# Performance work log

Measured on AMD Instinct MI355X. Metric: run time of the kernel, lower is better.

The kernel has to match this reference:

```python
import jax, jax.numpy as jnp
import numpy as np

B, T, H = 8, 2048, 2048

def glorot(key, shape):
    return jax.random.uniform(key, shape, minval=-1.0, maxval=1.0) * jnp.sqrt(2 / sum(shape))

def setup_inputs() -> dict:
    key = jax.random.key(0)
    kx, kr, ka, kb = jax.random.split(key, 4)
    x_seq = jax.random.normal(kx, (B, T, H), dtype=jnp.float32)
    reset = jax.random.randint(kr, (B, T), 0, 2).astype(bool)
    a_mat = glorot(ka, (H, H))
    b_mat = glorot(kb, (H, H))
    return {"x_seq": x_seq, "reset": reset, "a_mat": a_mat, "b_mat": b_mat}

def reference(x_seq, reset, a_mat, b_mat):
    # Precompute B^T x_t for all timesteps in one big GEMM: (B^T x)_k = sum_h b[h,k] x[h]
    bx = jnp.einsum('hk,bth->btk', b_mat, x_seq)  # [B,T,H]
    bx_t = jnp.swapaxes(bx, 0, 1)                 # [T,B,H] time-major
    reset_t = jnp.swapaxes(reset, 0, 1)           # [T,B]

    def step(h, inp):
        bx_step, r = inp                          # [B,H], [B]
        h = jnp.where(r[:, None], 0.0, h)         # reset hidden state
        h = h @ a_mat.T + bx_step                 # A @ h per batch row
        return h, h

    h0 = jnp.zeros((B, H), dtype=x_seq.dtype)
    _, h_seq = jax.lax.scan(step, h0, (bx_t, reset_t))
    return jnp.swapaxes(h_seq, 0, 1)              # [B,T,H]
```

## Files before the change

kernel.cpp:

```cpp
#include <hip/hip_runtime.h>

#define Hn 2048
#define Bn 8
#define Tn 2048
#define Cn 16
#define NCn (Tn / Cn)
#define M2n (NCn * Bn)

using f32x4 = __attribute__((ext_vector_type(4))) float;
using u32x4 = __attribute__((ext_vector_type(4))) unsigned int;
using us4   = __attribute__((ext_vector_type(4))) unsigned short;
using bf8   = __attribute__((ext_vector_type(8))) short;
using f4    = __attribute__((ext_vector_type(4))) float;

#define GLOAD16(g, l) __builtin_amdgcn_global_load_lds(                      \
    (const __attribute__((address_space(1))) void*)(g),                      \
    (__attribute__((address_space(3))) void*)(l), 16, 0, 0)

__device__ __forceinline__ unsigned short f2bf(float f) {
    unsigned u = __builtin_bit_cast(unsigned, f);
    u = u + 0x7fffu + ((u >> 16) & 1u);
    return (unsigned short)(u >> 16);
}
__device__ __forceinline__ float bf2f(unsigned short h) {
    unsigned u = ((unsigned)h) << 16;
    return __builtin_bit_cast(float, u);
}
__device__ __forceinline__ void split2f(float v, unsigned short& a, unsigned short& b) {
    a = f2bf(v);
    b = f2bf(v - bf2f(a));
}

__global__ __launch_bounds__(256) void k_reset_prep(const unsigned int* __restrict__ rin,
                                                    unsigned char* __restrict__ r8,
                                                    int* __restrict__ cut,
                                                    int* __restrict__ firstReset,
                                                    int* __restrict__ anyUncut,
                                                    int* __restrict__ perm,
                                                    int* __restrict__ iperm,
                                                    int* __restrict__ counts) {
    __shared__ int s_badInt, s_badFloat;
    __shared__ int hist[17], off[18], cur[17];
    if (threadIdx.x == 0) { s_badInt = 0; s_badFloat = 0; *anyUncut = 0; }
    if (threadIdx.x < 17) hist[threadIdx.x] = 0;
    __syncthreads();
    int badI = 0, badF = 0;
    for (int i = threadIdx.x; i < 4096; i += 256) {
        unsigned int v = rin[i];
        if (v > 1u) badI = 1;
        if (v != 0u && v != 0x3f800000u) badF = 1;
    }
    if (badI) atomicOr(&s_badInt, 1);
    if (badF) atomicOr(&s_badFloat, 1);
    __syncthreads();
    const int fmt = (!s_badInt) ? 0 : ((!s_badFloat) ? 1 : 2);
    const unsigned char* rb = (const unsigned char*)rin;
    const float* rf = (const float*)rin;
    for (int i = threadIdx.x; i < Bn * Tn; i += 256) {
        unsigned char v;
        if (fmt == 0)      v = (unsigned char)(rin[i] != 0u);
        else if (fmt == 1) v = (unsigned char)(rf[i] != 0.0f);
        else               v = (unsigned char)(rb[i] != 0);
        r8[i] = v;
    }
    __syncthreads();
    int anyU = 0;
    for (int m = threadIdx.x; m < M2n; m += 256) {
        int c = m / Bn, b = m % Bn;
        int fr = Cn;
        for (int j = 0; j < Cn; j++) {
            if (r8[b * Tn + c * Cn + j]) { fr = j; break; }
        }
        firstReset[m] = fr;
        int ct = (fr < Cn);
        cut[m] = ct;
        if (!ct && c < NCn - 1) anyU = 1;
        atomicAdd(&hist[fr], 1);
    }
    if (anyU) atomicOr(anyUncut, 1);
    __syncthreads();
    if (threadIdx.x == 0) {
        off[16] = 0;
        for (int v = 15; v >= 0; v--) off[v] = off[v + 1] + hist[v + 1];
        for (int v = 0; v < 17; v++) cur[v] = (v == 16) ? 0 : off[v];
        for (int j = 0; j < 16; j++) counts[j] = off[j];
    }
    __syncthreads();
    for (int m = threadIdx.x; m < M2n; m += 256) {
        int fr = firstReset[m];
        int pos = atomicAdd(&cur[fr], 1);
        perm[pos] = m;
        iperm[m] = pos;
    }
}

__global__ __launch_bounds__(256) void k_split_A2(const float* __restrict__ A,
                                                  unsigned short* __restrict__ a1,
                                                  unsigned short* __restrict__ a2) {
    size_t i = ((size_t)blockIdx.x * 256 + threadIdx.x) * 4;
    f32x4 v = *(const f32x4*)&A[i];
    us4 h1, h2;
#pragma unroll
    for (int e = 0; e < 4; e++) {
        unsigned short x1, x2;
        split2f(v[e], x1, x2);
        h1[e] = x1; h2[e] = x2;
    }
    *(us4*)&a1[i] = h1; *(us4*)&a2[i] = h2;
}

__global__ __launch_bounds__(256) void k_split_Bt(const float* __restrict__ Bm,
                                                  unsigned short* __restrict__ b1,
                                                  unsigned short* __restrict__ b2) {
    __shared__ float tile[64][65];
    const int k0 = blockIdx.y * 64, n0 = blockIdx.x * 64;
    const int c = threadIdx.x & 63, r4 = threadIdx.x >> 6;
#pragma unroll
    for (int i = 0; i < 16; i++) {
        int r = r4 * 16 + i;
        tile[r][c] = Bm[(size_t)(k0 + r) * Hn + n0 + c];
    }
    __syncthreads();
#pragma unroll
    for (int i = 0; i < 16; i++) {
        int r = r4 * 16 + i;
        float v = tile[c][r];
        unsigned short x1, x2;
        split2f(v, x1, x2);
        b1[(size_t)(n0 + r) * Hn + k0 + c] = x1;
        b2[(size_t)(n0 + r) * Hn + k0 + c] = x2;
    }
}

__global__ __launch_bounds__(256) void k_split_X(const float* __restrict__ X,
                                                 unsigned short* __restrict__ x1,
                                                 unsigned short* __restrict__ x2) {
    size_t i = ((size_t)blockIdx.x * 256 + threadIdx.x) * 4;
    f32x4 v = *(const f32x4*)&X[i];
    us4 h1, h2;
#pragma unroll
    for (int e = 0; e < 4; e++) {
        unsigned short a, b;
        split2f(v[e], a, b);
        h1[e] = a; h2[e] = b;
    }
    *(us4*)&x1[i] = h1; *(us4*)&x2[i] = h2;
}

template<int PREX>
__global__ __launch_bounds__(512) void k_gemm_p1(const unsigned short* __restrict__ X0,
                                                 const unsigned short* __restrict__ X1,
                                                 const unsigned short* __restrict__ B0,
                                                 const unsigned short* __restrict__ B1,
                                                 const float* __restrict__ Xf,
                                                 float* __restrict__ Out,
                                                 unsigned short* __restrict__ S0,
                                                 unsigned short* __restrict__ S1) {
    constexpr int BM = 256, BN = 128, LW = 32;
    __shared__ unsigned short ldsA[2 * BM * LW];
    __shared__ unsigned short ldsB[2 * BN * LW];
    const int tid = threadIdx.x;
    const int lane = tid & 63;
    const int wv = tid >> 6;
    const int wm = wv >> 1, wn = wv & 1;
    const int n0 = blockIdx.x * BN;
    const int m0 = blockIdx.y * BM;

    f4 acc[4][4];
#pragma unroll
    for (int fm = 0; fm < 4; fm++)
#pragma unroll
        for (int fn = 0; fn < 4; fn++) acc[fm][fn] = (f4){0.f, 0.f, 0.f, 0.f};

    const unsigned short* gA[4];
    unsigned short* lA[4];
    const float* gX[2];
    unsigned short* lX[2];
    const unsigned short* gB[2];
    unsigned short* lB[2];
    if constexpr (PREX) {
#pragma unroll
        for (int q = 0; q < 4; q++) {
            int u = tid + q * 512;
            int sp = u >> 10, row = (u >> 2) & 255, slot = u & 3;
            int g = slot ^ ((row >> 1) & 3);
            gA[q] = (sp ? X1 : X0) + (size_t)(m0 + row) * Hn + g * 8;
            lA[q] = &ldsA[u * 8];
        }
    } else {
#pragma unroll
        for (int q = 0; q < 2; q++) {
            int u = tid + q * 512;
            int row = u >> 2, slot = u & 3;
            int s = slot ^ ((row >> 1) & 3);
            gX[q] = Xf + (size_t)row * 0 + (size_t)(m0 + row) * Hn + slot * 8;
            lX[q] = &ldsA[row * LW + s * 8];
        }
    }
#pragma unroll
    for (int q = 0; q < 2; q++) {
        int u = tid + q * 512;
        int sp = u >> 9, row = (u >> 2) & 127, slot = u & 3;
        int g = slot ^ ((row >> 1) & 3);
        gB[q] = (sp ? B1 : B0) + (size_t)(n0 + row) * Hn + g * 8;
        lB[q] = &ldsB[u * 8];
    }
    const int sl = (lane >> 4) ^ ((lane >> 1) & 3);

    for (int k0 = 0; k0 < Hn; k0 += 32) {
        if constexpr (PREX) {
#pragma unroll
            for (int q = 0; q < 4; q++) {
                GLOAD16(gA[q], lA[q]);
                gA[q] += 32;
            }
        } else {
#pragma unroll
            for (int q = 0; q < 2; q++) {
                f32x4 va = *(const f32x4*)gX[q];
                f32x4 vb = *(const f32x4*)(gX[q] + 4);
                gX[q] += 32;
                us4 h1a, h2a, h1b, h2b;
#pragma unroll
                for (int e = 0; e < 4; e++) {
                    unsigned short p, r;
                    split2f(va[e], p, r); h1a[e] = p; h2a[e] = r;
                    split2f(vb[e], p, r); h1b[e] = p; h2b[e] = r;
                }
                *(us4*)lX[q] = h1a;
                *(us4*)(lX[q] + 4) = h1b;
                *(us4*)(lX[q] + BM * LW) = h2a;
                *(us4*)(lX[q] + BM * LW + 4) = h2b;
            }
        }
#pragma unroll
        for (int q = 0; q < 2; q++) {
            GLOAD16(gB[q], lB[q]);
            gB[q] += 32;
        }
        __syncthreads();

        bf8 af[2][4], bfr[2][4];
#pragma unroll
        for (int sp = 0; sp < 2; sp++)
#pragma unroll
            for (int f = 0; f < 4; f++)
                af[sp][f] = *(const bf8*)&ldsA[(sp * BM + wm * 64 + f * 16 + (lane & 15)) * LW + sl * 8];
#pragma unroll
        for (int sp = 0; sp < 2; sp++)
#pragma unroll
            for (int f = 0; f < 4; f++)
                bfr[sp][f] = *(const bf8*)&ldsB[(sp * BN + wn * 64 + f * 16 + (lane & 15)) * LW + sl * 8];

        const int pa[3] = {0, 0, 1};
        const int pb[3] = {0, 1, 0};
#pragma unroll
        for (int p = 0; p < 3; p++)
#pragma unroll
            for (int fm = 0; fm < 4; fm++)
#pragma unroll
                for (int fn = 0; fn < 4; fn++)
                    acc[fm][fn] = __builtin_amdgcn_mfma_f32_16x16x32_bf16(
                        af[pa[p]][fm], bfr[pb[p]][fn], acc[fm][fn], 0, 0, 0);
        __syncthreads();
    }

#pragma unroll
    for (int fm = 0; fm < 4; fm++)
#pragma unroll
        for (int r = 0; r < 4; r++) {
            int row = m0 + wm * 64 + fm * 16 + (lane >> 4) * 4 + r;
            int bb = row >> 11, t = row & 2047;
            int isC0 = ((t & 15) == 0);
            size_t ob = (size_t)row * Hn;
            size_t sb = (size_t)((t >> 4) * 8 + bb) * Hn;
#pragma unroll
            for (int fn = 0; fn < 4; fn++) {
                int n = n0 + wn * 64 + fn * 16 + (lane & 15);
                float v = acc[fm][fn][r];
                Out[ob + n] = v;
                if (isC0) {
                    unsigned short h1, h2;
                    split2f(v, h1, h2);
                    S0[sb + n] = h1; S1[sb + n] = h2;
                }
            }
        }
}

template<int PHASE>
__global__ __launch_bounds__(256) void k_gemm_s(const unsigned short* __restrict__ S0,
                                                const unsigned short* __restrict__ S1,
                                                const unsigned short* __restrict__ W0,
                                                const unsigned short* __restrict__ W1,
                                                float* __restrict__ Out,
                                                unsigned short* __restrict__ O0,
                                                unsigned short* __restrict__ O1,
                                                const unsigned char* __restrict__ r8v,
                                                const int* __restrict__ perm,
                                                const int* __restrict__ iperm,
                                                const int* __restrict__ counts,
                                                unsigned short* __restrict__ U0,
                                                unsigned short* __restrict__ U1,
                                                float* __restrict__ Hin,
                                                int j) {
    constexpr int BM = 64, BN = 64, BK = 64;
    __shared__ unsigned short ldsA[2 * BM * BK];
    __shared__ unsigned short ldsB[2 * BN * BK];
    const int tid = threadIdx.x;
    const int lane = tid & 63;
    const int wv = tid >> 6;
    const int wm = wv >> 1, wn = wv & 1;
    const int n0 = blockIdx.x * BN;
    const int m0 = blockIdx.y * BM;

    int cnt = 0;
    if constexpr (PHASE == 4) {
        cnt = counts[j];
        if (m0 >= cnt) return;
    }

    f4 acc[2][2];
#pragma unroll
    for (int fm = 0; fm < 2; fm++)
#pragma unroll
        for (int fn = 0; fn < 2; fn++) acc[fm][fn] = (f4){0.f, 0.f, 0.f, 0.f};

    const unsigned short* gA[4];
    unsigned short* lA[4];
    const unsigned short* gB[4];
    unsigned short* lB[4];
#pragma unroll
    for (int q = 0; q < 4; q++) {
        int u = tid + q * 256;
        int sp = u >> 9, row = (u >> 3) & 63, s = u & 7;
        int g = s ^ (row & 7);
        gA[q] = (sp ? S1 : S0) + (size_t)(m0 + row) * Hn + g * 8;
        lA[q] = &ldsA[u * 8];
        gB[q] = (sp ? W1 : W0) + (size_t)(n0 + row) * Hn + g * 8;
        lB[q] = &ldsB[u * 8];
    }

    for (int k0 = 0; k0 < Hn; k0 += BK) {
#pragma unroll
        for (int q = 0; q < 4; q++) {
            GLOAD16(gA[q], lA[q]);
            GLOAD16(gB[q], lB[q]);
            gA[q] += BK;
            gB[q] += BK;
        }
        __syncthreads();

        const int pa[3] = {0, 0, 1};
        const int pb[3] = {0, 1, 0};
#pragma unroll
        for (int h = 0; h < 2; h++) {
            const int sl = (h * 4 + (lane >> 4)) ^ (lane & 7);
            bf8 af[2][2], bfr[2][2];
#pragma unroll
            for (int sp = 0; sp < 2; sp++)
#pragma unroll
                for (int f = 0; f < 2; f++) {
                    af[sp][f] = *(const bf8*)&ldsA[(sp * BM + wm * 32 + f * 16 + (lane & 15)) * BK + sl * 8];
                    bfr[sp][f] = *(const bf8*)&ldsB[(sp * BN + wn * 32 + f * 16 + (lane & 15)) * BK + sl * 8];
                }
#pragma unroll
            for (int p = 0; p < 3; p++)
#pragma unroll
                for (int fm = 0; fm < 2; fm++)
#pragma unroll
                    for (int fn = 0; fn < 2; fn++)
                        acc[fm][fn] = __builtin_amdgcn_mfma_f32_16x16x32_bf16(
                            af[pa[p]][fm], bfr[pb[p]][fn], acc[fm][fn], 0, 0, 0);
        }
        __syncthreads();
    }

    if constexpr (PHASE == 2 || PHASE == 3) {
#pragma unroll
        for (int fm = 0; fm < 2; fm++)
#pragma unroll
            for (int r = 0; r < 4; r++) {
                int m = m0 + wm * 32 + fm * 16 + (lane >> 4) * 4 + r;
                int cch = m >> 3, bb = m & 7;
                int t = cch * Cn + j;
                int rfl = r8v[bb * Tn + t];
                size_t ob = ((size_t)bb * Tn + t) * (size_t)Hn;
                size_t sb = (size_t)m * Hn;
                int carry = 0;
                size_t ub = 0, hb = 0;
                if constexpr (PHASE == 3) {
                    carry = (m < M2n - 8);
                    if (carry) {
                        ub = (size_t)iperm[m + 8] * Hn;
                        hb = (size_t)(m + 8) * Hn;
                    }
                }
#pragma unroll
                for (int fn = 0; fn < 2; fn++) {
                    int n = n0 + wn * 32 + fn * 16 + (lane & 15);
                    float v = (rfl ? 0.0f : acc[fm][fn][r]) + Out[ob + n];
                    Out[ob + n] = v;
                    unsigned short h1, h2;
                    split2f(v, h1, h2);
                    O0[sb + n] = h1; O1[sb + n] = h2;
                    if constexpr (PHASE == 3) {
                        if (carry) {
                            U0[ub + n] = h1; U1[ub + n] = h2;
                            Hin[hb + n] = v;
                        }
                    }
                }
            }
    } else {
#pragma unroll
        for (int fm = 0; fm < 2; fm++)
#pragma unroll
            for (int r = 0; r < 4; r++) {
                int s = m0 + wm * 32 + fm * 16 + (lane >> 4) * 4 + r;
                int alive = (s < cnt);
                int m = perm[s];
                int cch = m >> 3, bb = m & 7;
                int t = cch * Cn + j;
                size_t ob = ((size_t)bb * Tn + t) * (size_t)Hn;
                size_t sb = (size_t)s * Hn;
#pragma unroll
                for (int fn = 0; fn < 2; fn++) {
                    int n = n0 + wn * 32 + fn * 16 + (lane & 15);
                    if (alive) {
                        float val = acc[fm][fn][r];
                        unsigned short h1, h2;
                        split2f(val, h1, h2);
                        O0[sb + n] = h1; O1[sb + n] = h2;
                        Out[ob + n] += val;
                    }
                }
            }
    }
}

__global__ __launch_bounds__(256) void k_zero_c0(const int* __restrict__ iperm,
                                                 unsigned short* __restrict__ U0,
                                                 unsigned short* __restrict__ U1,
                                                 float* __restrict__ Hin) {
    int b = blockIdx.x;
    int s = iperm[b];
    for (int n = threadIdx.x; n < Hn; n += 256) {
        U0[(size_t)s * Hn + n] = 0;
        U1[(size_t)s * Hn + n] = 0;
        Hin[(size_t)b * Hn + n] = 0.0f;
    }
}

__global__ __launch_bounds__(1024) void k_fallback(float* __restrict__ Hin,
                                                   const float* __restrict__ A,
                                                   const int* __restrict__ cut,
                                                   const int* __restrict__ anyUncut,
                                                   unsigned short* __restrict__ u1,
                                                   unsigned short* __restrict__ u2,
                                                   const int* __restrict__ iperm) {
    if (*anyUncut == 0) return;
    __shared__ float v0[Hn];
    __shared__ float v1[Hn];
    for (int c = 1; c < NCn; c++) {
        for (int b = 0; b < Bn; b++) {
            if (cut[(c - 1) * Bn + b]) continue;
            for (int n = threadIdx.x; n < Hn; n += 1024)
                v0[n] = Hin[((size_t)(c - 1) * Bn + b) * Hn + n];
            __syncthreads();
            for (int s = 0; s < Cn; s++) {
                float* pin = (s & 1) ? v1 : v0;
                float* pout = (s & 1) ? v0 : v1;
                for (int n = threadIdx.x; n < Hn; n += 1024) {
                    float accv = 0.0f;
                    const float* Ar = &A[(size_t)n * Hn];
                    for (int k = 0; k < Hn; k++) accv += pin[k] * Ar[k];
                    pout[n] = accv;
                }
                __syncthreads();
            }
            float* pres = (Cn & 1) ? v1 : v0;
            int mrow = c * Bn + b;
            size_t dst = (size_t)mrow * Hn;
            size_t sdst = (size_t)iperm[mrow] * Hn;
            for (int n = threadIdx.x; n < Hn; n += 1024) {
                float nv = Hin[dst + n] + pres[n];
                Hin[dst + n] = nv;
                unsigned short h1, h2;
                split2f(nv, h1, h2);
                u1[sdst + n] = h1; u2[sdst + n] = h2;
            }
            __syncthreads();
        }
    }
}

extern "C" void kernel_launch(void* const* d_in, const int* in_sizes, int n_in,
                              void* d_out, int out_size, void* d_ws, size_t ws_size,
                              hipStream_t stream) {
    const float* x = (const float*)d_in[0];
    const unsigned int* rst = (const unsigned int*)d_in[1];
    const float* Am = (const float*)d_in[2];
    const float* Bm = (const float*)d_in[3];
    float* Out = (float*)d_out;
    char* ws = (char*)d_ws;

    unsigned char* r8 = (unsigned char*)ws;
    int* cut = (int*)(ws + 16384);
    int* firstReset = (int*)(ws + 20480);
    int* perm = (int*)(ws + 24576);
    int* iperm = (int*)(ws + 28672);
    int* counts = (int*)(ws + 32768);
    int* anyUncut = (int*)(ws + 32832);
    unsigned short* a1 = (unsigned short*)(ws + 65536);
    unsigned short* a2 = a1 + 4194304;
    unsigned short* b1 = a2 + 4194304;
    unsigned short* b2 = b1 + 4194304;
    unsigned short* sP1 = b2 + 4194304;
    unsigned short* sP2 = sP1 + 2097152;
    unsigned short* sQ1 = sP2 + 2097152;
    unsigned short* sQ2 = sQ1 + 2097152;
    unsigned short* uP1 = sQ2 + 2097152;
    unsigned short* uP2 = uP1 + 2097152;
    float* Hin = (float*)(uP2 + 2097152);
    unsigned short* x1 = (unsigned short*)(Hin + 2097152);
    unsigned short* x2 = x1 + 33554432;
    const size_t NEED_X = 201392128ull;
    const bool prex = (ws_size >= NEED_X);

    k_reset_prep<<<1, 256, 0, stream>>>(rst, r8, cut, firstReset, anyUncut, perm, iperm, counts);
    k_split_A2<<<4096, 256, 0, stream>>>(Am, a1, a2);
    k_split_Bt<<<dim3(32, 32), 256, 0, stream>>>(Bm, b1, b2);

    if (prex) {
        k_split_X<<<32768, 256, 0, stream>>>(x, x1, x2);
        k_gemm_p1<1><<<dim3(Hn / 128, (Bn * Tn) / 256), 512, 0, stream>>>(
            x1, x2, b1, b2, nullptr, Out, sP1, sP2);
    } else {
        k_gemm_p1<0><<<dim3(Hn / 128, (Bn * Tn) / 256), 512, 0, stream>>>(
            nullptr, nullptr, b1, b2, x, Out, sP1, sP2);
    }

    for (int j = 1; j < Cn; j++) {
        const unsigned short* i1 = (j & 1) ? sP1 : sQ1;
        const unsigned short* i2 = (j & 1) ? sP2 : sQ2;
        unsigned short* o1 = (j & 1) ? sQ1 : sP1;
        unsigned short* o2 = (j & 1) ? sQ2 : sP2;
        if (j < Cn - 1) {
            k_gemm_s<2><<<dim3(Hn / 64, M2n / 64), 256, 0, stream>>>(
                i1, i2, a1, a2, Out, o1, o2, r8, nullptr, nullptr, nullptr,
                nullptr, nullptr, nullptr, j);
        } else {
            k_gemm_s<3><<<dim3(Hn / 64, M2n / 64), 256, 0, stream>>>(
                i1, i2, a1, a2, Out, o1, o2, r8, nullptr, iperm, nullptr,
                uP1, uP2, Hin, j);
        }
    }

    k_zero_c0<<<8, 256, 0, stream>>>(iperm, uP1, uP2, Hin);
    k_fallback<<<1, 1024, 0, stream>>>(Hin, Am, cut, anyUncut, uP1, uP2, iperm);

    for (int j = 0; j < Cn; j++) {
        const unsigned short* i1 = (j == 0) ? uP1 : ((j & 1) ? sP1 : sQ1);
        const unsigned short* i2 = (j == 0) ? uP2 : ((j & 1) ? sP2 : sQ2);
        unsigned short* o1 = (j & 1) ? sQ1 : sP1;
        unsigned short* o2 = (j & 1) ? sQ2 : sP2;
        k_gemm_s<4><<<dim3(Hn / 64, M2n / 64), 256, 0, stream>>>(
            i1, i2, a1, a2, Out, o1, o2, nullptr, perm, nullptr, counts,
            nullptr, nullptr, nullptr, j);
    }
}
```

Before: 1.349 ms.

## Overlap global-to-LDS loads with MFMA in GEMM kernels via prefetch and double buffering

In the big precomputed-input GEMM, fragments are read from LDS into registers, then the next K-tile's global_load_lds is issued before the MFMAs so the load overlaps compute with a single buffer. The chunked GEMM kernel k_gemm_s gets a two-stage double buffer with waits on the vector-memory counter, so tile t+2 loads while tile t is computed. This hides memory latency but adds LDS usage (double in k_gemm_s) and register pressure from holding both K halves of fragments, which could lower occupancy.

Result: faster. 1.288 ms (-4.5%).

```diff
diff --git a/kernel.cpp b/kernel.cpp
--- a/kernel.cpp
+++ b/kernel.cpp
@@ -193,7 +193,7 @@
             int u = tid + q * 512;
             int row = u >> 2, slot = u & 3;
             int s = slot ^ ((row >> 1) & 3);
-            gX[q] = Xf + (size_t)row * 0 + (size_t)(m0 + row) * Hn + slot * 8;
+            gX[q] = Xf + (size_t)(m0 + row) * Hn + slot * 8;
             lX[q] = &ldsA[row * LW + s * 8];
         }
     }
@@ -206,15 +206,54 @@
         lB[q] = &ldsB[u * 8];
     }
     const int sl = (lane >> 4) ^ ((lane >> 1) & 3);
-
-    for (int k0 = 0; k0 < Hn; k0 += 32) {
-        if constexpr (PREX) {
-#pragma unroll
-            for (int q = 0; q < 4; q++) {
-                GLOAD16(gA[q], lA[q]);
-                gA[q] += 32;
-            }
-        } else {
+    const int pa[3] = {0, 0, 1};
+    const int pb[3] = {0, 1, 0};
+
+    if constexpr (PREX) {
+#pragma unroll
+        for (int q = 0; q < 4; q++) { GLOAD16(gA[q], lA[q]); gA[q] += 32; }
+#pragma unroll
+        for (int q = 0; q < 2; q++) { GLOAD16(gB[q], lB[q]); gB[q] += 32; }
+
+        for (int k0 = 0; k0 < Hn; k0 += 32) {
+            asm volatile("s_waitcnt vmcnt(0)" ::: "memory");
+            __builtin_amdgcn_sched_barrier(0);
+            __builtin_amdgcn_s_barrier();
+
+            bf8 af[2][4], bfr[2][4];
+#pragma unroll
+            for (int sp = 0; sp < 2; sp++)
+#pragma unroll
+                for (int f = 0; f < 4; f++)
+                    af[sp][f] = *(const bf8*)&ldsA[(sp * BM + wm * 64 + f * 16 + (lane & 15)) * LW + sl * 8];
+#pragma unroll
+            for (int sp = 0; sp < 2; sp++)
+#pragma unroll
+                for (int f = 0; f < 4; f++)
+                    bfr[sp][f] = *(const bf8*)&ldsB[(sp * BN + wn * 64 + f * 16 + (lane & 15)) * LW + sl * 8];
+            asm volatile("s_waitcnt lgkmcnt(0)" ::: "memory");
+            __builtin_amdgcn_sched_barrier(0);
+            __builtin_amdgcn_s_barrier();
+
+            if (k0 + 32 < Hn) {
+#pragma unroll
+                for (int q = 0; q < 4; q++) { GLOAD16(gA[q], lA[q]); gA[q] += 32; }
+#pragma unroll
+                for (int q = 0; q < 2; q++) { GLOAD16(gB[q], lB[q]); gB[q] += 32; }
+            }
+            __builtin_amdgcn_sched_barrier(0);
+
+#pragma unroll
+            for (int p = 0; p < 3; p++)
+#pragma unroll
+                for (int fm = 0; fm < 4; fm++)
+#pragma unroll
+                    for (int fn = 0; fn < 4; fn++)
+                        acc[fm][fn] = __builtin_amdgcn_mfma_f32_16x16x32_bf16(
+                            af[pa[p]][fm], bfr[pb[p]][fn], acc[fm][fn], 0, 0, 0);
+        }
+    } else {
+        for (int k0 = 0; k0 < Hn; k0 += 32) {
 #pragma unroll
             for (int q = 0; q < 2; q++) {
                 f32x4 va = *(const f32x4*)gX[q];
@@ -232,37 +271,34 @@
                 *(us4*)(lX[q] + BM * LW) = h2a;
                 *(us4*)(lX[q] + BM * LW + 4) = h2b;
             }
-        }
-#pragma unroll
-        for (int q = 0; q < 2; q++) {
-            GLOAD16(gB[q], lB[q]);
-            gB[q] += 32;
-        }
-        __syncthreads();
-
-        bf8 af[2][4], bfr[2][4];
-#pragma unroll
-        for (int sp = 0; sp < 2; sp++)
-#pragma unroll
-            for (int f = 0; f < 4; f++)
-                af[sp][f] = *(const bf8*)&ldsA[(sp * BM + wm * 64 + f * 16 + (lane & 15)) * LW + sl * 8];
-#pragma unroll
-        for (int sp = 0; sp < 2; sp++)
-#pragma unroll
-            for (int f = 0; f < 4; f++)
-                bfr[sp][f] = *(const bf8*)&ldsB[(sp * BN + wn * 64 + f * 16 + (lane & 15)) * LW + sl * 8];
-
-        const int pa[3] = {0, 0, 1};
-        const int pb[3] = {0, 1, 0};
-#pragma unroll
-        for (int p = 0; p < 3; p++)
-#pragma unroll
-            for (int fm = 0; fm < 4; fm++)
-#pragma unroll
-                for (int fn = 0; fn < 4; fn++)
-                    acc[fm][fn] = __builtin_amdgcn_mfma_f32_16x16x32_bf16(
-                        af[pa[p]][fm], bfr[pb[p]][fn], acc[fm][fn], 0, 0, 0);
-        __syncthreads();
+#pragma unroll
+            for (int q = 0; q < 2; q++) {
+                GLOAD16(gB[q], lB[q]);
+                gB[q] += 32;
+            }
+            __syncthreads();
+
+            bf8 af[2][4], bfr[2][4];
+#pragma unroll
+            for (int sp = 0; sp < 2; sp++)
+#pragma unroll
+                for (int f = 0; f < 4; f++)
+                    af[sp][f] = *(const bf8*)&ldsA[(sp * BM + wm * 64 + f * 16 + (lane & 15)) * LW + sl * 8];
+#pragma unroll
+            for (int sp = 0; sp < 2; sp++)
+#pragma unroll
+                for (int f = 0; f < 4; f++)
+                    bfr[sp][f] = *(const bf8*)&ldsB[(sp * BN + wn * 64 + f * 16 + (lane & 15)) * LW + sl * 8];
+#pragma unroll
+            for (int p = 0; p < 3; p++)
+#pragma unroll
+                for (int fm = 0; fm < 4; fm++)
+#pragma unroll
+                    for (int fn = 0; fn < 4; fn++)
+                        acc[fm][fn] = __builtin_amdgcn_mfma_f32_16x16x32_bf16(
+                            af[pa[p]][fm], bfr[pb[p]][fn], acc[fm][fn], 0, 0, 0);
+            __syncthreads();
+        }
     }
 
 #pragma unroll
@@ -305,8 +341,10 @@
                                                 float* __restrict__ Hin,
                                                 int j) {
     constexpr int BM = 64, BN = 64, BK = 64;
-    __shared__ unsigned short ldsA[2 * BM * BK];
-    __shared__ unsigned short ldsB[2 * BN * BK];
+    constexpr int TSZ = 2 * BM * BK;
+    constexpr int NT = Hn / BK;
+    __shared__ unsigned short ldsA[2 * TSZ];
+    __shared__ unsigned short ldsB[2 * TSZ];
     const int tid = threadIdx.x;
     const int lane = tid & 63;
     const int wv = tid >> 6;
@@ -340,30 +378,52 @@
         gB[q] = (sp ? W1 : W0) + (size_t)(n0 + row) * Hn + g * 8;
         lB[q] = &ldsB[u * 8];
     }
-
-    for (int k0 = 0; k0 < Hn; k0 += BK) {
-#pragma unroll
-        for (int q = 0; q < 4; q++) {
-            GLOAD16(gA[q], lA[q]);
-            GLOAD16(gB[q], lB[q]);
-            gA[q] += BK;
-            gB[q] += BK;
-        }
-        __syncthreads();
-
-        const int pa[3] = {0, 0, 1};
-        const int pb[3] = {0, 1, 0};
+    const int pa[3] = {0, 0, 1};
+    const int pb[3] = {0, 1, 0};
+
+#define STAGE_S(bsel)                                                        \
+    {                                                                        \
+        const int boff_ = (bsel) * TSZ;                                      \
+        _Pragma("unroll")                                                    \
+        for (int q = 0; q < 4; q++) {                                        \
+            GLOAD16(gA[q], lA[q] + boff_);                                   \
+            GLOAD16(gB[q], lB[q] + boff_);                                   \
+            gA[q] += BK; gB[q] += BK;                                        \
+        }                                                                    \
+    }
+
+    STAGE_S(0);
+    STAGE_S(1);
+
+    for (int t = 0; t < NT; t++) {
+        if (t == NT - 1) { asm volatile("s_waitcnt vmcnt(0)" ::: "memory"); }
+        else             { asm volatile("s_waitcnt vmcnt(8)" ::: "memory"); }
+        __builtin_amdgcn_sched_barrier(0);
+        __builtin_amdgcn_s_barrier();
+
+        const unsigned short* curA = &ldsA[(t & 1) * TSZ];
+        const unsigned short* curB = &ldsB[(t & 1) * TSZ];
+        bf8 af[2][2][2], bfr[2][2][2];
 #pragma unroll
         for (int h = 0; h < 2; h++) {
-            const int sl = (h * 4 + (lane >> 4)) ^ (lane & 7);
-            bf8 af[2][2], bfr[2][2];
+            const int slh = ((h * 4) + (lane >> 4)) ^ (lane & 7);
 #pragma unroll
             for (int sp = 0; sp < 2; sp++)
 #pragma unroll
                 for (int f = 0; f < 2; f++) {
-                    af[sp][f] = *(const bf8*)&ldsA[(sp * BM + wm * 32 + f * 16 + (lane & 15)) * BK + sl * 8];
-                    bfr[sp][f] = *(const bf8*)&ldsB[(sp * BN + wn * 32 + f * 16 + (lane & 15)) * BK + sl * 8];
+                    af[h][sp][f] = *(const bf8*)&curA[(sp * BM + wm * 32 + f * 16 + (lane & 15)) * BK + slh * 8];
+                    bfr[h][sp][f] = *(const bf8*)&curB[(sp * BN + wn * 32 + f * 16 + (lane & 15)) * BK + slh * 8];
                 }
+        }
+        asm volatile("s_waitcnt lgkmcnt(0)" ::: "memory");
+        __builtin_amdgcn_sched_barrier(0);
+        __builtin_amdgcn_s_barrier();
+
+        if (t + 2 < NT) STAGE_S(t & 1);
+        __builtin_amdgcn_sched_barrier(0);
+
+#pragma unroll
+        for (int h = 0; h < 2; h++)
 #pragma unroll
             for (int p = 0; p < 3; p++)
 #pragma unroll
@@ -371,10 +431,9 @@
 #pragma unroll
                     for (int fn = 0; fn < 2; fn++)
                         acc[fm][fn] = __builtin_amdgcn_mfma_f32_16x16x32_bf16(
-                            af[pa[p]][fm], bfr[pb[p]][fn], acc[fm][fn], 0, 0, 0);
-        }
-        __syncthreads();
-    }
+                            af[h][pa[p]][fm], bfr[h][pb[p]][fn], acc[fm][fn], 0, 0, 0);
+    }
+#undef STAGE_S
 
     if constexpr (PHASE == 2 || PHASE == 3) {
 #pragma unroll
```
